# Optimization experiments

Measured on AMD Instinct MI355X. Metric: run time of the kernel, lower is better.

Reference implementation:

```python
import jax, jax.numpy as jnp
import numpy as np

MARGIN_POS = 0.0
MARGIN_NEG = 1.0
NUM_CLASSES = 1000


def setup_inputs() -> dict:
    key = jax.random.key(0)
    k1, k2, k3, k4, k5 = jax.random.split(key, 5)
    B, D, M = 1024, 512, 32768
    R = M - B  # memory bank length after dedup/truncate
    embeddings = jax.random.normal(k1, (B, D), dtype=jnp.float32)
    labels = jax.random.randint(k2, (B,), 0, NUM_CLASSES).astype(jnp.int64)
    emb_mem = jax.random.normal(k3, (R, D), dtype=jnp.float32)
    # offset so memory labels are disjoint from batch labels (torch.isin dedup is a no-op)
    lbl_mem = (jax.random.randint(k4, (R,), 0, NUM_CLASSES) + NUM_CLASSES).astype(jnp.int64)
    add_to_mem = jax.random.randint(k5, (B,), 0, 2).astype(bool)
    return {"embeddings": embeddings, "labels": labels, "emb_mem": emb_mem,
            "lbl_mem": lbl_mem, "add_to_mem": add_to_mem}


def _loss(embeddings, labels, emb_mem, lbl_mem):
    B = embeddings.shape[0]
    # reference set = detached batch embeddings ++ memory bank (both are constants w.r.t. grad)
    ref_e = jax.lax.stop_gradient(jnp.concatenate([embeddings, emb_mem], axis=0))  # [R, D]
    ref_l = jnp.concatenate([labels, lbl_mem], axis=0)                              # [R]
    idx_ref = jnp.concatenate([jnp.arange(B, dtype=labels.dtype),
                               -jnp.ones(lbl_mem.shape[0], dtype=labels.dtype)])    # [R]
    # squared L2 distance matrix [B, R] via (|a|^2 + |b|^2 - 2 a.b), clamped at 0
    sq_a = jnp.sum(embeddings * embeddings, axis=1)  # [B]
    sq_b = jnp.sum(ref_e * ref_e, axis=1)            # [R]
    d = jnp.maximum(sq_a[:, None] + sq_b[None, :] - 2.0 * (embeddings @ ref_e.T), 0.0)
    not_self = idx_ref[None, :] != jnp.arange(B, dtype=labels.dtype)[:, None]  # [B, R]
    same = labels[:, None] == ref_l[None, :]                                   # [B, R]
    loss_ap = d - MARGIN_POS
    loss_an = jnp.maximum(MARGIN_NEG - d, 0.0)
    mask_pos = same & not_self & (loss_ap > 0)
    mask_neg = (~same) & not_self & (loss_an > 0)
    eps = 1e-6
    loss_pos = (jnp.where(mask_pos, loss_ap, 0.0).sum(1)
                / (mask_pos.sum(1).astype(d.dtype) + eps)).sum()
    loss_neg = (jnp.where(mask_neg, loss_an, 0.0).sum(1)
                / (mask_neg.sum(1).astype(d.dtype) + eps)).sum()
    return (loss_pos + loss_neg) / B


def reference(embeddings, labels, emb_mem, lbl_mem, add_to_mem):
    # add_to_mem only affects the (stateful) memory-bank update, not the returned loss
    return _loss(embeddings, labels, emb_mem, lbl_mem)
```

## Files before the change

### kernel.cpp

```cpp
#include <hip/hip_runtime.h>

typedef __attribute__((ext_vector_type(8))) short short8;
typedef __attribute__((ext_vector_type(4))) float f32x4;

#define GLOAD16(g, l)                                                        \
  __builtin_amdgcn_global_load_lds(                                          \
      (const __attribute__((address_space(1))) unsigned int*)(g),            \
      (__attribute__((address_space(3))) unsigned int*)(l), 16, 0, 0)

__device__ __forceinline__ unsigned short f2bf(float f) {
  union { float f; unsigned int u; } v;
  v.f = f;
  unsigned int u = v.u;
  u += 0x7FFFu + ((u >> 16) & 1u);
  return (unsigned short)(u >> 16);
}

__device__ __forceinline__ short8 pack8(float4 a, float4 b) {
  short8 r;
  r[0] = (short)f2bf(a.x); r[1] = (short)f2bf(a.y);
  r[2] = (short)f2bf(a.z); r[3] = (short)f2bf(a.w);
  r[4] = (short)f2bf(b.x); r[5] = (short)f2bf(b.y);
  r[6] = (short)f2bf(b.z); r[7] = (short)f2bf(b.w);
  return r;
}

__global__ __launch_bounds__(256)
void prep2_kernel(const float* __restrict__ emb, const int* __restrict__ labels,
                  const float* __restrict__ emb_mem, const int* __restrict__ lbl_mem,
                  unsigned short* __restrict__ refbf, float* __restrict__ sqb,
                  int* __restrict__ reflab, int Bn, int Dn, int Mn) {
  int wid = threadIdx.x >> 6, lane = threadIdx.x & 63;
  int row = blockIdx.x * 4 + wid;
  if (row >= Mn) return;
  const float* src = (row < Bn) ? (emb + (size_t)row * Dn)
                                : (emb_mem + (size_t)(row - Bn) * Dn);
  unsigned short* dst = refbf + (size_t)row * Dn;
  float s = 0.f;
  for (int c0 = lane * 8; c0 < Dn; c0 += 64 * 8) {
    float4 v0 = ((const float4*)(src + c0))[0];
    float4 v1 = ((const float4*)(src + c0))[1];
    s += v0.x * v0.x + v0.y * v0.y + v0.z * v0.z + v0.w * v0.w;
    s += v1.x * v1.x + v1.y * v1.y + v1.z * v1.z + v1.w * v1.w;
    *(short8*)(dst + c0) = pack8(v0, v1);
  }
#pragma unroll
  for (int off = 32; off; off >>= 1) s += __shfl_xor(s, off);
  if (lane == 0) {
    sqb[row] = s;
    reflab[row] = (row < Bn) ? labels[row] : lbl_mem[row - Bn];
  }
}

#define BM 128
#define BN 128
#define BK 32

__global__ __launch_bounds__(256)
void gemm_epi_kernel(const unsigned short* __restrict__ refbf,
                     const float* __restrict__ sqb,
                     const int* __restrict__ reflab,
                     float* __restrict__ part,
                     int Dn, int mtiles, int ntiles) {
  __shared__ unsigned short As[BM * BK];
  __shared__ unsigned short Bs[BN * BK];
  __shared__ float redbuf[2 * BM * 4];

  int bid = blockIdx.x;
  int it, jt;
  if (mtiles == 8 && (ntiles & 7) == 0) {
    int c = bid & 7, g = bid >> 3;
    int per = ntiles >> 3;
    jt = c * per + (g >> 3);
    it = g & 7;
  } else {
    it = bid % mtiles;
    jt = bid / mtiles;
  }
  int rowBase = it * BM;
  int colBase = jt * BN;

  int tid = threadIdx.x, lane = tid & 63, w = tid >> 6;
  int wr = w >> 1, wc = w & 1;
  int l16 = lane & 15, quad = lane >> 4;

  int lrow = lane >> 2, lk = lane & 3;
  size_t rowB = (size_t)Dn * 2;
  int r0 = w * 32 + lrow;
  int ca = (lk - (r0 >> 1)) & 3;
  const char* gA0 = (const char*)refbf + (size_t)(rowBase + r0) * rowB + ca * 16;
  const char* gA1 = gA0 + 16 * rowB;
  const char* gB0 = (const char*)refbf + (size_t)(colBase + r0) * rowB + ca * 16;
  const char* gB1 = gB0 + 16 * rowB;
  char* lA = (char*)As + w * 2048;
  char* lB = (char*)Bs + w * 2048;

  f32x4 acc[4][4] = {};

  for (int k0 = 0; k0 < Dn; k0 += BK) {
    int koff = k0 * 2;
    GLOAD16(gA0 + koff, lA);
    GLOAD16(gA1 + koff, lA + 1024);
    GLOAD16(gB0 + koff, lB);
    GLOAD16(gB1 + koff, lB + 1024);
    __syncthreads();

    short8 af[4], bfr[4];
#pragma unroll
    for (int mi = 0; mi < 4; ++mi) {
      int row = wr * 64 + mi * 16 + l16;
      af[mi] = *(const short8*)&As[row * BK + ((quad + (row >> 1)) & 3) * 8];
    }
#pragma unroll
    for (int ni = 0; ni < 4; ++ni) {
      int row = wc * 64 + ni * 16 + l16;
      bfr[ni] = *(const short8*)&Bs[row * BK + ((quad + (row >> 1)) & 3) * 8];
    }
#pragma unroll
    for (int mi = 0; mi < 4; ++mi)
#pragma unroll
      for (int ni = 0; ni < 4; ++ni)
        acc[mi][ni] = __builtin_amdgcn_mfma_f32_16x16x32_bf16(
            af[mi], bfr[ni], acc[mi][ni], 0, 0, 0);
    __syncthreads();
  }

  float sqc[4];
  int labc[4];
#pragma unroll
  for (int ni = 0; ni < 4; ++ni) {
    int gcol = colBase + wc * 64 + ni * 16 + l16;
    sqc[ni] = sqb[gcol];
    labc[ni] = reflab[gcol];
  }
#pragma unroll
  for (int mi = 0; mi < 4; ++mi) {
    int lr0 = wr * 64 + mi * 16 + quad * 4;
#pragma unroll
    for (int r = 0; r < 4; ++r) {
      int lrow_loc = lr0 + r;
      int grow = rowBase + lrow_loc;
      float sqr = sqb[grow];
      int labr = reflab[grow];
      float ps = 0.f, pc = 0.f, ns = 0.f, nc = 0.f;
#pragma unroll
      for (int ni = 0; ni < 4; ++ni) {
        int gcol = colBase + wc * 64 + ni * 16 + l16;
        float dist = sqr + sqc[ni] - 2.0f * acc[mi][ni][r];
        dist = fmaxf(dist, 0.f);
        bool self = (gcol == grow);
        bool same = (labc[ni] == labr);
        if (same && !self && dist > 0.f) { ps += dist; pc += 1.f; }
        if (!same && !self && dist < 1.f) { ns += 1.f - dist; nc += 1.f; }
      }
#pragma unroll
      for (int off = 8; off; off >>= 1) {
        ps += __shfl_xor(ps, off);
        pc += __shfl_xor(pc, off);
        ns += __shfl_xor(ns, off);
        nc += __shfl_xor(nc, off);
      }
      if (l16 == 0) {
        f32x4 v = {ps, pc, ns, nc};
        *(f32x4*)&redbuf[(wc * BM + lrow_loc) * 4] = v;
      }
    }
  }
  __syncthreads();
  size_t slab = ((size_t)jt * mtiles + it) * (BM * 4);
  part[slab + tid]       = redbuf[tid]       + redbuf[BM * 4 + tid];
  part[slab + 256 + tid] = redbuf[256 + tid] + redbuf[BM * 4 + 256 + tid];
}

__global__ __launch_bounds__(256)
void reduce_rows_kernel(const float* __restrict__ part,
                        float* __restrict__ rowloss,
                        int mtiles, int ntiles, int Bn) {
  int wid = threadIdx.x >> 6, lane = threadIdx.x & 63;
  int row = blockIdx.x * 4 + wid;
  if (row >= Bn) return;
  int it = row / BM, lr = row % BM;
  f32x4 a = {0.f, 0.f, 0.f, 0.f};
  for (int jt = lane; jt < ntiles; jt += 64) {
    f32x4 v = *(const f32x4*)&part[((size_t)jt * mtiles + it) * (BM * 4) + lr * 4];
    a[0] += v[0]; a[1] += v[1]; a[2] += v[2]; a[3] += v[3];
  }
#pragma unroll
  for (int off = 32; off; off >>= 1) {
    a[0] += __shfl_xor(a[0], off);
    a[1] += __shfl_xor(a[1], off);
    a[2] += __shfl_xor(a[2], off);
    a[3] += __shfl_xor(a[3], off);
  }
  if (lane == 0)
    rowloss[row] = a[0] / (a[1] + 1e-6f) + a[2] / (a[3] + 1e-6f);
}

__global__ void finalize_kernel(const float* __restrict__ rowloss,
                                float* __restrict__ out, int Bn) {
  __shared__ float red[4];
  int tid = threadIdx.x;
  float v = 0.f;
  for (int i = tid; i < Bn; i += 256) v += rowloss[i];
#pragma unroll
  for (int off = 32; off; off >>= 1) v += __shfl_xor(v, off);
  if ((tid & 63) == 0) red[tid >> 6] = v;
  __syncthreads();
  if (tid == 0) out[0] = (red[0] + red[1] + red[2] + red[3]) / (float)Bn;
}

extern "C" void kernel_launch(void* const* d_in, const int* in_sizes, int n_in,
                              void* d_out, int out_size, void* d_ws, size_t ws_size,
                              hipStream_t stream) {
  const float* emb     = (const float*)d_in[0];
  const int*   labels  = (const int*)d_in[1];
  const float* emb_mem = (const float*)d_in[2];
  const int*   lbl_mem = (const int*)d_in[3];

  int Bn = in_sizes[1];
  int Dn = in_sizes[0] / Bn;
  int Rn = in_sizes[3];
  int Mn = Bn + Rn;
  int mtiles = Bn / BM, ntiles = Mn / BN;

  char* ws = (char*)d_ws;
  unsigned short* refbf = (unsigned short*)ws;
  size_t off = (size_t)Mn * Dn * 2;
  float* sqb    = (float*)(ws + off);
  int*   reflab = (int*)(ws + off + (size_t)Mn * 4);
  float* part   = (float*)(ws + off + (size_t)Mn * 8);
  float* rowloss= part + (size_t)ntiles * mtiles * (BM * 4);

  prep2_kernel<<<(Mn + 3) / 4, 256, 0, stream>>>(
      emb, labels, emb_mem, lbl_mem, refbf, sqb, reflab, Bn, Dn, Mn);

  gemm_epi_kernel<<<mtiles * ntiles, 256, 0, stream>>>(
      refbf, sqb, reflab, part, Dn, mtiles, ntiles);

  reduce_rows_kernel<<<(Bn + 3) / 4, 256, 0, stream>>>(
      part, rowloss, mtiles, ntiles, Bn);

  finalize_kernel<<<1, 256, 0, stream>>>(rowloss, (float*)d_out, Bn);
}
```

Before: 177.8 us.

## Specialize GEMM for D=512, shorten epilogue reduction, fuse final reductions

Adds a GEMM kernel specialised for D=512 with a fully unrolled K loop and constant row strides. Its epilogue packs the positive and negative counts into one float and uses a single shuffle step plus an LDS reduction, cutting shuffles. Partials are now stored row-major so the row reduction reads contiguously. The row reduce and finalize kernels are merged into one kernel that finishes with an atomic counter, removing a launch but relying on atomics and a reset done inside prep.

```diff
diff --git a/kernel.cpp b/kernel.cpp
--- a/kernel.cpp
+++ b/kernel.cpp
@@ -25,11 +25,17 @@
   return r;
 }
 
+#define BM 128
+#define BN 128
+#define BK 32
+
 __global__ __launch_bounds__(256)
 void prep2_kernel(const float* __restrict__ emb, const int* __restrict__ labels,
                   const float* __restrict__ emb_mem, const int* __restrict__ lbl_mem,
                   unsigned short* __restrict__ refbf, float* __restrict__ sqb,
-                  int* __restrict__ reflab, int Bn, int Dn, int Mn) {
+                  int* __restrict__ reflab, float* __restrict__ facc,
+                  int* __restrict__ fcnt, int Bn, int Dn, int Mn) {
+  if (blockIdx.x == 0 && threadIdx.x == 0) { *facc = 0.f; *fcnt = 0; }
   int wid = threadIdx.x >> 6, lane = threadIdx.x & 63;
   int row = blockIdx.x * 4 + wid;
   if (row >= Mn) return;
@@ -52,38 +58,132 @@
   }
 }
 
-#define BM 128
-#define BN 128
-#define BK 32
-
 __global__ __launch_bounds__(256)
-void gemm_epi_kernel(const unsigned short* __restrict__ refbf,
-                     const float* __restrict__ sqb,
-                     const int* __restrict__ reflab,
-                     float* __restrict__ part,
-                     int Dn, int mtiles, int ntiles) {
-  __shared__ unsigned short As[BM * BK];
-  __shared__ unsigned short Bs[BN * BK];
-  __shared__ float redbuf[2 * BM * 4];
-
+void gemm512_kernel(const unsigned short* __restrict__ refbf,
+                    const float* __restrict__ sqb,
+                    const int* __restrict__ reflab,
+                    float* __restrict__ part) {
+  __shared__ __align__(16) char smem[32768];
+  unsigned short* As = (unsigned short*)smem;
+  unsigned short* Bs = (unsigned short*)(smem + 8192);
+  f32x4* red4 = (f32x4*)smem;
+
+  const int ntiles = 256;
   int bid = blockIdx.x;
-  int it, jt;
-  if (mtiles == 8 && (ntiles & 7) == 0) {
-    int c = bid & 7, g = bid >> 3;
-    int per = ntiles >> 3;
-    jt = c * per + (g >> 3);
-    it = g & 7;
-  } else {
-    it = bid % mtiles;
-    jt = bid / mtiles;
-  }
-  int rowBase = it * BM;
-  int colBase = jt * BN;
+  int c = bid & 7, g = bid >> 3;
+  int jt = c * 32 + (g >> 3);
+  int it = g & 7;
+  int rowBase = it * BM, colBase = jt * BN;
 
   int tid = threadIdx.x, lane = tid & 63, w = tid >> 6;
   int wr = w >> 1, wc = w & 1;
   int l16 = lane & 15, quad = lane >> 4;
-
+  int lrow = lane >> 2, lk = lane & 3;
+  int r0 = w * 32 + lrow;
+  int ca = (lk - (r0 >> 1)) & 3;
+
+  const char* gA0 = (const char*)refbf + (size_t)(rowBase + r0) * 1024 + ca * 16;
+  const char* gA1 = gA0 + 16 * 1024;
+  const char* gB0 = (const char*)refbf + (size_t)(colBase + r0) * 1024 + ca * 16;
+  const char* gB1 = gB0 + 16 * 1024;
+  char* lA = (char*)As + w * 2048;
+  char* lB = (char*)Bs + w * 2048;
+
+  f32x4 acc[4][4] = {};
+#pragma unroll
+  for (int kk = 0; kk < 16; ++kk) {
+    GLOAD16(gA0 + kk * 64, lA);
+    GLOAD16(gA1 + kk * 64, lA + 1024);
+    GLOAD16(gB0 + kk * 64, lB);
+    GLOAD16(gB1 + kk * 64, lB + 1024);
+    __syncthreads();
+    short8 af[4], bfr[4];
+#pragma unroll
+    for (int mi = 0; mi < 4; ++mi) {
+      int row = wr * 64 + mi * 16 + l16;
+      af[mi] = *(const short8*)&As[row * BK + ((quad + (row >> 1)) & 3) * 8];
+    }
+#pragma unroll
+    for (int ni = 0; ni < 4; ++ni) {
+      int row = wc * 64 + ni * 16 + l16;
+      bfr[ni] = *(const short8*)&Bs[row * BK + ((quad + (row >> 1)) & 3) * 8];
+    }
+#pragma unroll
+    for (int mi = 0; mi < 4; ++mi)
+#pragma unroll
+      for (int ni = 0; ni < 4; ++ni)
+        acc[mi][ni] = __builtin_amdgcn_mfma_f32_16x16x32_bf16(
+            af[mi], bfr[ni], acc[mi][ni], 0, 0, 0);
+    __syncthreads();
+  }
+
+  float sqc[4];
+  int labc[4];
+#pragma unroll
+  for (int ni = 0; ni < 4; ++ni) {
+    int gcol = colBase + wc * 64 + ni * 16 + l16;
+    sqc[ni] = sqb[gcol];
+    labc[ni] = reflab[gcol];
+  }
+#pragma unroll
+  for (int mi = 0; mi < 4; ++mi) {
+    int lr0 = wr * 64 + mi * 16 + quad * 4;
+#pragma unroll
+    for (int r = 0; r < 4; ++r) {
+      int lrl = lr0 + r;
+      int grow = rowBase + lrl;
+      float sqr = sqb[grow];
+      int labr = reflab[grow];
+      float ps = 0.f, ns = 0.f, cpk = 0.f;
+#pragma unroll
+      for (int ni = 0; ni < 4; ++ni) {
+        int gcol = colBase + wc * 64 + ni * 16 + l16;
+        float dist = fmaxf(sqr + sqc[ni] - 2.0f * acc[mi][ni][r], 0.f);
+        bool self = (gcol == grow);
+        bool same = (labc[ni] == labr);
+        if (same && !self && dist > 0.f) { ps += dist; cpk += 1.f; }
+        if (!same && !self && dist < 1.f) { ns += 1.f - dist; cpk += 512.f; }
+      }
+      ps += __shfl_xor(ps, 8);
+      ns += __shfl_xor(ns, 8);
+      cpk += __shfl_xor(cpk, 8);
+      if (l16 < 8) {
+        f32x4 v = {ps, ns, cpk, 0.f};
+        red4[(wc * BM + lrl) * 8 + l16] = v;
+      }
+    }
+  }
+  __syncthreads();
+  if (tid < BM) {
+    f32x4 s = {0.f, 0.f, 0.f, 0.f};
+#pragma unroll
+    for (int c2 = 0; c2 < 2; ++c2)
+#pragma unroll
+      for (int k = 0; k < 8; ++k)
+        s += red4[(c2 * BM + tid) * 8 + ((k + tid) & 7)];
+    float nc = floorf(s[2] * (1.0f / 512.0f));
+    float pc = s[2] - 512.f * nc;
+    f32x4 o = {s[0], pc, s[1], nc};
+    ((f32x4*)part)[(size_t)(rowBase + tid) * ntiles + jt] = o;
+  }
+}
+
+__global__ __launch_bounds__(256)
+void gemm_generic_kernel(const unsigned short* __restrict__ refbf,
+                         const float* __restrict__ sqb,
+                         const int* __restrict__ reflab,
+                         float* __restrict__ part,
+                         int Dn, int mtiles, int ntiles) {
+  __shared__ unsigned short As[BM * BK];
+  __shared__ unsigned short Bs[BN * BK];
+  __shared__ f32x4 redbuf4[2 * BM];
+
+  int bid = blockIdx.x;
+  int it = bid % mtiles, jt = bid / mtiles;
+  int rowBase = it * BM, colBase = jt * BN;
+  int tid = threadIdx.x, lane = tid & 63, w = tid >> 6;
+  int wr = w >> 1, wc = w & 1;
+  int l16 = lane & 15, quad = lane >> 4;
   int lrow = lane >> 2, lk = lane & 3;
   size_t rowB = (size_t)Dn * 2;
   int r0 = w * 32 + lrow;
@@ -96,7 +196,6 @@
   char* lB = (char*)Bs + w * 2048;
 
   f32x4 acc[4][4] = {};
-
   for (int k0 = 0; k0 < Dn; k0 += BK) {
     int koff = k0 * 2;
     GLOAD16(gA0 + koff, lA);
@@ -104,7 +203,6 @@
     GLOAD16(gB0 + koff, lB);
     GLOAD16(gB1 + koff, lB + 1024);
     __syncthreads();
-
     short8 af[4], bfr[4];
 #pragma unroll
     for (int mi = 0; mi < 4; ++mi) {
@@ -138,16 +236,15 @@
     int lr0 = wr * 64 + mi * 16 + quad * 4;
 #pragma unroll
     for (int r = 0; r < 4; ++r) {
-      int lrow_loc = lr0 + r;
-      int grow = rowBase + lrow_loc;
+      int lrl = lr0 + r;
+      int grow = rowBase + lrl;
       float sqr = sqb[grow];
       int labr = reflab[grow];
       float ps = 0.f, pc = 0.f, ns = 0.f, nc = 0.f;
 #pragma unroll
       for (int ni = 0; ni < 4; ++ni) {
         int gcol = colBase + wc * 64 + ni * 16 + l16;
-        float dist = sqr + sqc[ni] - 2.0f * acc[mi][ni][r];
-        dist = fmaxf(dist, 0.f);
+        float dist = fmaxf(sqr + sqc[ni] - 2.0f * acc[mi][ni][r], 0.f);
         bool self = (gcol == grow);
         bool same = (labc[ni] == labr);
         if (same && !self && dist > 0.f) { ps += dist; pc += 1.f; }
@@ -162,51 +259,52 @@
       }
       if (l16 == 0) {
         f32x4 v = {ps, pc, ns, nc};
-        *(f32x4*)&redbuf[(wc * BM + lrow_loc) * 4] = v;
+        redbuf4[wc * BM + lrl] = v;
       }
     }
   }
   __syncthreads();
-  size_t slab = ((size_t)jt * mtiles + it) * (BM * 4);
-  part[slab + tid]       = redbuf[tid]       + redbuf[BM * 4 + tid];
-  part[slab + 256 + tid] = redbuf[256 + tid] + redbuf[BM * 4 + 256 + tid];
+  if (tid < BM) {
+    f32x4 s = redbuf4[tid] + redbuf4[BM + tid];
+    ((f32x4*)part)[(size_t)(rowBase + tid) * ntiles + jt] = s;
+  }
 }
 
 __global__ __launch_bounds__(256)
-void reduce_rows_kernel(const float* __restrict__ part,
-                        float* __restrict__ rowloss,
-                        int mtiles, int ntiles, int Bn) {
-  int wid = threadIdx.x >> 6, lane = threadIdx.x & 63;
-  int row = blockIdx.x * 4 + wid;
-  if (row >= Bn) return;
-  int it = row / BM, lr = row % BM;
-  f32x4 a = {0.f, 0.f, 0.f, 0.f};
-  for (int jt = lane; jt < ntiles; jt += 64) {
-    f32x4 v = *(const f32x4*)&part[((size_t)jt * mtiles + it) * (BM * 4) + lr * 4];
-    a[0] += v[0]; a[1] += v[1]; a[2] += v[2]; a[3] += v[3];
-  }
-#pragma unroll
-  for (int off = 32; off; off >>= 1) {
-    a[0] += __shfl_xor(a[0], off);
-    a[1] += __shfl_xor(a[1], off);
-    a[2] += __shfl_xor(a[2], off);
-    a[3] += __shfl_xor(a[3], off);
-  }
-  if (lane == 0)
-    rowloss[row] = a[0] / (a[1] + 1e-6f) + a[2] / (a[3] + 1e-6f);
-}
-
-__global__ void finalize_kernel(const float* __restrict__ rowloss,
-                                float* __restrict__ out, int Bn) {
-  __shared__ float red[4];
-  int tid = threadIdx.x;
-  float v = 0.f;
-  for (int i = tid; i < Bn; i += 256) v += rowloss[i];
-#pragma unroll
-  for (int off = 32; off; off >>= 1) v += __shfl_xor(v, off);
-  if ((tid & 63) == 0) red[tid >> 6] = v;
+void reduce_final_kernel(const float* __restrict__ part,
+                         float* __restrict__ facc, int* __restrict__ fcnt,
+                         float* __restrict__ out, int Bn, int ntiles) {
+  __shared__ float rsum[4];
+  int tid = threadIdx.x, w = tid >> 6, lane = tid & 63;
+  int row = blockIdx.x * 4 + w;
+  const f32x4* part4 = (const f32x4*)part;
+  float rl = 0.f;
+  if (row < Bn) {
+    f32x4 a = {0.f, 0.f, 0.f, 0.f};
+    for (int j = lane; j < ntiles; j += 64)
+      a += part4[(size_t)row * ntiles + j];
+#pragma unroll
+    for (int off = 32; off; off >>= 1) {
+      a[0] += __shfl_xor(a[0], off);
+      a[1] += __shfl_xor(a[1], off);
+      a[2] += __shfl_xor(a[2], off);
+      a[3] += __shfl_xor(a[3], off);
+    }
+    rl = a[0] / (a[1] + 1e-6f) + a[2] / (a[3] + 1e-6f);
+  }
+  if (lane == 0) rsum[w] = rl;
   __syncthreads();
-  if (tid == 0) out[0] = (red[0] + red[1] + red[2] + red[3]) / (float)Bn;
+  if (tid == 0) {
+    float bs = rsum[0] + rsum[1] + rsum[2] + rsum[3];
+    atomicAdd(facc, bs);
+    __threadfence();
+    int old = atomicAdd(fcnt, 1);
+    if (old == (int)gridDim.x - 1) {
+      __threadfence();
+      float tot = atomicAdd(facc, 0.f);
+      out[0] = tot / (float)Bn;
+    }
+  }
 }
 
 extern "C" void kernel_launch(void* const* d_in, const int* in_sizes, int n_in,
@@ -229,16 +327,19 @@
   float* sqb    = (float*)(ws + off);
   int*   reflab = (int*)(ws + off + (size_t)Mn * 4);
   float* part   = (float*)(ws + off + (size_t)Mn * 8);
-  float* rowloss= part + (size_t)ntiles * mtiles * (BM * 4);
+  float* facc   = part + (size_t)Bn * ntiles * 4;
+  int*   fcnt   = (int*)(facc + 1);
 
   prep2_kernel<<<(Mn + 3) / 4, 256, 0, stream>>>(
-      emb, labels, emb_mem, lbl_mem, refbf, sqb, reflab, Bn, Dn, Mn);
-
-  gemm_epi_kernel<<<mtiles * ntiles, 256, 0, stream>>>(
-      refbf, sqb, reflab, part, Dn, mtiles, ntiles);
-
-  reduce_rows_kernel<<<(Bn + 3) / 4, 256, 0, stream>>>(
-      part, rowloss, mtiles, ntiles, Bn);
-
-  finalize_kernel<<<1, 256, 0, stream>>>(rowloss, (float*)d_out, Bn);
-}
+      emb, labels, emb_mem, lbl_mem, refbf, sqb, reflab, facc, fcnt, Bn, Dn, Mn);
+
+  if (Dn == 512 && mtiles == 8 && ntiles == 256) {
+    gemm512_kernel<<<2048, 256, 0, stream>>>(refbf, sqb, reflab, part);
+  } else {
+    gemm_generic_kernel<<<mtiles * ntiles, 256, 0, stream>>>(
+        refbf, sqb, reflab, part, Dn, mtiles, ntiles);
+  }
+
+  reduce_final_kernel<<<(Bn + 3) / 4, 256, 0, stream>>>(
+      part, facc, fcnt, (float*)d_out, Bn, ntiles);
+}
```

After: 164.0 us. -7.8%, faster.
